# Optimization experiments

Hardware: AMD Instinct MI355X
Metric: run time of the kernel (lower is better)

## Reference

```python
import jax, jax.numpy as jnp
import numpy as np

B = 32768      # batch of graphs
H = 128        # hidden_channels
L = 3          # num message-passing layers
T = 3          # num_timesteps
NB, NJ = 1, 12 # base nodes, joint nodes
NN = NB + NJ   # 13 nodes per graph
OBS_W = 47     # obs features per timestep
BASE_IDX = np.array(list(range(9)) + [45, 46])   # 11 base features per timestep
JOINT_IDX = np.array(list(range(9, 45)))          # 36 joint features per timestep
BASE_F = T * len(BASE_IDX)                        # 33
JOINT_F = (len(JOINT_IDX) // NJ) * T              # 9

# fixed tree edges, both directions (24 edges per graph)
_n2n = np.array([[0, 0, 0, 0, 1, 2, 4, 5, 7, 8, 10, 11],
                 [1, 4, 7, 10, 2, 3, 5, 6, 8, 9, 11, 12]])
SRC = np.concatenate([_n2n[0], _n2n[1]])
DST = np.concatenate([_n2n[1], _n2n[0]])


def setup_inputs() -> dict:
    key = jax.random.key(0)
    ks = jax.random.split(key, 10)
    s = 0.05
    return {
        "obs": jax.random.normal(ks[0], (B, T * OBS_W), dtype=jnp.float32),
        "We_b": jax.random.normal(ks[1], (H, BASE_F), dtype=jnp.float32) * s,
        "be_b": jax.random.normal(ks[2], (H,), dtype=jnp.float32) * s,
        "We_j": jax.random.normal(ks[3], (H, JOINT_F), dtype=jnp.float32) * s,
        "be_j": jax.random.normal(ks[4], (H,), dtype=jnp.float32) * s,
        "W_rel": jax.random.normal(ks[5], (L, H, H), dtype=jnp.float32) * s,
        "W_root": jax.random.normal(ks[6], (L, H, H), dtype=jnp.float32) * s,
        "b_rel": jax.random.normal(ks[7], (L, H), dtype=jnp.float32) * s,
        "W_dec": jax.random.normal(ks[8], (1, H), dtype=jnp.float32) * s,
        "b_dec": jax.random.normal(ks[9], (1,), dtype=jnp.float32) * s,
        "src": jnp.asarray(SRC, dtype=jnp.int32),
        "dst": jnp.asarray(DST, dtype=jnp.int32),
    }


def reference(obs, We_b, be_b, We_j, be_j, W_rel, W_root, b_rel, W_dec, b_dec, src, dst):
    b = obs.shape[0]
    elu = jax.nn.elu
    # ---- obs -> per-node features ----
    obs3 = obs[:, :T * OBS_W].reshape(b, T, OBS_W)
    base_feat = obs3[:, :, BASE_IDX].reshape(b, NB, BASE_F)                 # [B,1,33]
    joint_feat = (obs3[:, :, JOINT_IDX]
                  .reshape(b, T, len(JOINT_IDX) // NJ, NJ)
                  .transpose(0, 3, 1, 2)
                  .reshape(b, NJ, JOINT_F))                                  # [B,12,9]
    # ---- encoders ----
    xb = elu(jnp.einsum('bnf,hf->bnh', base_feat, We_b) + be_b)
    xj = elu(jnp.einsum('bnf,hf->bnh', joint_feat, We_j) + be_j)
    x = jnp.concatenate([xb, xj], axis=1)                                    # [B,13,H]
    # ---- GraphConv layers: out = W_root x + W_rel (scatter_add of x_src at dst) + b ----
    for l in range(L):
        agg = jnp.zeros_like(x).at[:, dst].add(x[:, src])                    # [B,13,H]
        x = elu(jnp.einsum('bnh,oh->bno', agg, W_rel[l]) + b_rel[l]
                + jnp.einsum('bnh,oh->bno', x, W_root[l]))
    # ---- per-joint decoder ----
    out = jnp.einsum('bnh,oh->bno', x[:, NB:], W_dec) + b_dec                # [B,12,1]
    return out.reshape(b, NJ)
```

## Files before the change

kernel.cpp:

```cpp
#include <hip/hip_runtime.h>

#define H      128
#define OBSROW 141
#define GPB    16
#define NT     256

typedef __bf16 bf16x8 __attribute__((ext_vector_type(8)));
typedef float  f32x4  __attribute__((ext_vector_type(4)));

__device__ __forceinline__ float eluf(float v) {
    return v > 0.0f ? v : (__expf(v) - 1.0f);
}
__device__ __forceinline__ f32x4 mf(bf16x8 a, bf16x8 b, f32x4 c) {
    return __builtin_amdgcn_mfma_f32_16x16x32_bf16(a, b, c, 0, 0, 0);
}
__device__ __forceinline__ void store_pk4(unsigned short* dst, f32x4 a) {
    union { unsigned short u[4]; unsigned long long v; } pk;
    #pragma unroll
    for (int r = 0; r < 4; r++) {
        __bf16 b = (__bf16)eluf(a[r]);
        pk.u[r] = *(unsigned short*)&b;
    }
    *(unsigned long long*)dst = pk.v;
}

#define WS_ROOT 49152
#define WS_EB   98304
#define WS_EJ   106496
#define WS_TOT  110592

__global__ void convert_weights(const float* __restrict__ Wr, const float* __restrict__ Wo,
                                const float* __restrict__ Web, const float* __restrict__ Wej,
                                __bf16* __restrict__ ws) {
    const int i = blockIdx.x * 256 + threadIdx.x;
    if (i < WS_ROOT) {
        ws[i] = (__bf16)Wr[i];
    } else if (i < WS_EB) {
        ws[i] = (__bf16)Wo[i - WS_ROOT];
    } else if (i < WS_EJ) {
        const int j = i - WS_EB, o = j >> 6, f = j & 63;
        ws[i] = (__bf16)(f < 33 ? Web[o*33 + f] : 0.0f);
    } else if (i < WS_TOT) {
        const int j = i - WS_EJ, o = j >> 5, f = j & 31;
        ws[i] = (__bf16)(f < 9 ? Wej[o*9 + f] : 0.0f);
    }
}

#define XIDX(n,hc,g,hi) (((((n)*16 + (hc))*16 + (g))*8) + (hi))

__launch_bounds__(NT, 2)
__global__ void gnn_fused(const float* __restrict__ obs,
                          const float* __restrict__ be_b, const float* __restrict__ be_j,
                          const float* __restrict__ b_rel,
                          const float* __restrict__ W_dec, const float* __restrict__ b_dec,
                          const __bf16* __restrict__ wsb,
                          float* __restrict__ out, int B)
{
    __shared__ __align__(16) unsigned short Xs[13*2048];
    __shared__ __align__(16) unsigned short Fs[7168];

    const int tid  = threadIdx.x;
    const int wave = tid >> 6;
    const int lane = tid & 63;
    const int q    = lane >> 4;
    const int c    = lane & 15;
    const int g0   = blockIdx.x * GPB;

    static constexpr int ODEG[13]    = {4,2,2,1,2,2,1,2,2,1,2,2,1};
    static constexpr int ODST[13][4] = {
        {1,4,7,10},{0,2,0,0},{1,3,0,0},{2,0,0,0},{0,5,0,0},{4,6,0,0},{5,0,0,0},
        {0,8,0,0},{7,9,0,0},{8,0,0,0},{0,11,0,0},{10,12,0,0},{11,0,0,0}};

    const int hcs0 = wave*4 + (q>>1);
    const int wofs = c*8 + (q&1)*4;

    {
        float* raw = (float*)Xs;
        for (int i = tid; i < GPB*OBSROW; i += NT) {
            const int g = i / OBSROW;
            raw[i] = ((g0 + g) < B) ? obs[(g0+g)*OBSROW + (i - g*OBSROW)] : 0.0f;
        }
    }
    __syncthreads();

    {
        const float* raw = (const float*)Xs;
        for (int s = tid; s < 6144; s += NT) {
            const int jj = s >> 9, rem = s & 511;
            const int fc = rem >> 7, g = (rem >> 3) & 15, hi = rem & 7;
            const int f = fc*8 + hi;
            float v = 0.0f;
            if (f < 9)
                v = raw[g*OBSROW + (f/3)*47 + 9 + (f%3)*12 + jj];
            *(__bf16*)&Fs[s] = (__bf16)v;
        }
        for (int s = tid; s < 1024; s += NT) {
            const int fc = s >> 7, rem = s & 127, g = rem >> 3, hi = rem & 7;
            const int f = fc*8 + hi;
            float v = 0.0f;
            if (f < 33) {
                const int tt = f / 11, i2 = f % 11;
                v = raw[g*OBSROW + tt*47 + (i2 < 9 ? i2 : 36 + i2)];
            }
            *(__bf16*)&Fs[6144 + s] = (__bf16)v;
        }
    }
    __syncthreads();

    {
        const int orow = wave*32 + c;
        const bf16x8 a0 = *(const bf16x8*)&Fs[6144 + q*128 + c*8];
        const bf16x8 a1 = *(const bf16x8*)&Fs[6144 + 512 + q*128 + c*8];
        #pragma unroll
        for (int s = 0; s < 2; s++) {
            const bf16x8 u0 = *(const bf16x8*)(wsb + WS_EB + (orow + s*16)*64 + q*8);
            const bf16x8 u1 = *(const bf16x8*)(wsb + WS_EB + (orow + s*16)*64 + 32 + q*8);
            const float4 b4 = *(const float4*)&be_b[wave*32 + s*16 + q*4];
            f32x4 acc = {b4.x, b4.y, b4.z, b4.w};
            acc = mf(u0, a0, acc);
            acc = mf(u1, a1, acc);
            store_pk4(&Xs[(hcs0 + s*2)*128 + wofs], acc);
        }
        #pragma unroll
        for (int s = 0; s < 2; s++) {
            const bf16x8 uj = *(const bf16x8*)(wsb + WS_EJ + (orow + s*16)*32 + q*8);
            const float4 b4 = *(const float4*)&be_j[wave*32 + s*16 + q*4];
            const f32x4 bias = {b4.x, b4.y, b4.z, b4.w};
            #pragma unroll
            for (int jj = 0; jj < 12; jj++) {
                const bf16x8 a = *(const bf16x8*)&Fs[jj*512 + q*128 + c*8];
                f32x4 acc = bias;
                acc = mf(uj, a, acc);
                store_pk4(&Xs[(1+jj)*2048 + (hcs0 + s*2)*128 + wofs], acc);
            }
        }
    }
    __syncthreads();

    const unsigned short* xb_base = Xs + q*128 + c*8;
    #pragma unroll 1
    for (int l = 0; l < 3; l++) {
        const __bf16* wr = wsb + l*16384;
        const __bf16* wo = wsb + WS_ROOT + l*16384;
        bf16x8 Wr[2][4], Wt[2][4];
        #pragma unroll
        for (int s = 0; s < 2; s++) {
            const int row = (wave*32 + s*16 + c)*128 + q*8;
            #pragma unroll
            for (int ks = 0; ks < 4; ks++) {
                Wr[s][ks] = *(const bf16x8*)(wr + row + ks*32);
                Wt[s][ks] = *(const bf16x8*)(wo + row + ks*32);
            }
        }
        f32x4 acc[13][2];
        #pragma unroll
        for (int s = 0; s < 2; s++) {
            const float4 b4 = *(const float4*)&b_rel[l*H + wave*32 + s*16 + q*4];
            const f32x4 bias = {b4.x, b4.y, b4.z, b4.w};
            #pragma unroll
            for (int n = 0; n < 13; n++) acc[n][s] = bias;
        }
        #pragma unroll
        for (int n = 0; n < 13; n++) {
            bf16x8 xb[4];
            #pragma unroll
            for (int ks = 0; ks < 4; ks++)
                xb[ks] = *(const bf16x8*)(xb_base + n*2048 + ks*512);
            f32x4 y0 = {0.f,0.f,0.f,0.f}, y1 = {0.f,0.f,0.f,0.f};
            #pragma unroll
            for (int ks = 0; ks < 4; ks++) {
                acc[n][0] = mf(Wt[0][ks], xb[ks], acc[n][0]);
                acc[n][1] = mf(Wt[1][ks], xb[ks], acc[n][1]);
                y0 = mf(Wr[0][ks], xb[ks], y0);
                y1 = mf(Wr[1][ks], xb[ks], y1);
            }
            #pragma unroll
            for (int e = 0; e < 4; e++)
                if (e < ODEG[n]) {
                    acc[ODST[n][e]][0] += y0;
                    acc[ODST[n][e]][1] += y1;
                }
        }
        __syncthreads();
        #pragma unroll
        for (int n = 0; n < 13; n++) {
            store_pk4(&Xs[n*2048 +  hcs0     *128 + wofs], acc[n][0]);
            store_pk4(&Xs[n*2048 + (hcs0 + 2)*128 + wofs], acc[n][1]);
        }
        __syncthreads();
    }

    {
        const unsigned short* xdec = Xs + q*512 + c*8;
        float wd[32];
        #pragma unroll
        for (int i4 = 0; i4 < 8; i4++) {
            const float4 wv = *(const float4*)&W_dec[q*32 + i4*4];
            wd[i4*4+0] = wv.x; wd[i4*4+1] = wv.y; wd[i4*4+2] = wv.z; wd[i4*4+3] = wv.w;
        }
        const float bd = b_dec[0];
        for (int j = wave; j < 12; j += 4) {
            float s = 0.0f;
            #pragma unroll
            for (int hq = 0; hq < 4; hq++) {
                const bf16x8 xv = *(const bf16x8*)(xdec + (j+1)*2048 + hq*128);
                #pragma unroll
                for (int hi2 = 0; hi2 < 8; hi2++)
                    s += (float)xv[hi2] * wd[hq*8 + hi2];
            }
            s += __shfl_xor(s, 16);
            s += __shfl_xor(s, 32);
            if (q == 0 && (g0 + c) < B)
                out[(g0 + c)*12 + j] = s + bd;
        }
    }
}

extern "C" void kernel_launch(void* const* d_in, const int* in_sizes, int n_in,
                              void* d_out, int out_size, void* d_ws, size_t ws_size,
                              hipStream_t stream) {
    const float* obs   = (const float*)d_in[0];
    const float* We_b  = (const float*)d_in[1];
    const float* be_b  = (const float*)d_in[2];
    const float* We_j  = (const float*)d_in[3];
    const float* be_j  = (const float*)d_in[4];
    const float* W_rel = (const float*)d_in[5];
    const float* W_root= (const float*)d_in[6];
    const float* b_rel = (const float*)d_in[7];
    const float* W_dec = (const float*)d_in[8];
    const float* b_dec = (const float*)d_in[9];
    float* out = (float*)d_out;
    __bf16* wsb = (__bf16*)d_ws;

    const int B = in_sizes[0] / OBSROW;
    convert_weights<<<(WS_TOT + 255) / 256, 256, 0, stream>>>(W_rel, W_root, We_b, We_j, wsb);
    const int blocks = (B + GPB - 1) / GPB;
    gnn_fused<<<blocks, NT, 0, stream>>>(obs, be_b, be_j, b_rel, W_dec, b_dec,
                                         wsb, out, B);
}
```

Baseline: 208.5 us.

## Alias feature staging buffer into node buffer to allow three blocks per CU

Drops the separate feature LDS buffer and stages the encoder inputs inside the tail of the node-feature buffer, lowering shared memory per block. Launch bounds go from 2 to 3 blocks per CU so more blocks can be resident. Because the joint encoder outputs for the last nodes overlap the staging area, their results are kept in registers, an extra barrier is added, and they are written back afterwards. The costs are higher register pressure from the held accumulators and a tighter register budget under the new launch bound, which may cause spills.

```diff
diff --git a/kernel.cpp b/kernel.cpp
--- a/kernel.cpp
+++ b/kernel.cpp
@@ -46,9 +46,9 @@
     }
 }
 
-#define XIDX(n,hc,g,hi) (((((n)*16 + (hc))*16 + (g))*8) + (hi))
-
-__launch_bounds__(NT, 2)
+#define G0U 19456
+
+__launch_bounds__(NT, 3)
 __global__ void gnn_fused(const float* __restrict__ obs,
                           const float* __restrict__ be_b, const float* __restrict__ be_j,
                           const float* __restrict__ b_rel,
@@ -57,7 +57,6 @@
                           float* __restrict__ out, int B)
 {
     __shared__ __align__(16) unsigned short Xs[13*2048];
-    __shared__ __align__(16) unsigned short Fs[7168];
 
     const int tid  = threadIdx.x;
     const int wave = tid >> 6;
@@ -92,7 +91,7 @@
             float v = 0.0f;
             if (f < 9)
                 v = raw[g*OBSROW + (f/3)*47 + 9 + (f%3)*12 + jj];
-            *(__bf16*)&Fs[s] = (__bf16)v;
+            *(__bf16*)&Xs[G0U + s] = (__bf16)v;
         }
         for (int s = tid; s < 1024; s += NT) {
             const int fc = s >> 7, rem = s & 127, g = rem >> 3, hi = rem & 7;
@@ -102,15 +101,15 @@
                 const int tt = f / 11, i2 = f % 11;
                 v = raw[g*OBSROW + tt*47 + (i2 < 9 ? i2 : 36 + i2)];
             }
-            *(__bf16*)&Fs[6144 + s] = (__bf16)v;
+            *(__bf16*)&Xs[G0U + 6144 + s] = (__bf16)v;
         }
     }
     __syncthreads();
 
     {
         const int orow = wave*32 + c;
-        const bf16x8 a0 = *(const bf16x8*)&Fs[6144 + q*128 + c*8];
-        const bf16x8 a1 = *(const bf16x8*)&Fs[6144 + 512 + q*128 + c*8];
+        const bf16x8 a0 = *(const bf16x8*)&Xs[G0U + 6144 + q*128 + c*8];
+        const bf16x8 a1 = *(const bf16x8*)&Xs[G0U + 6144 + 512 + q*128 + c*8];
         #pragma unroll
         for (int s = 0; s < 2; s++) {
             const bf16x8 u0 = *(const bf16x8*)(wsb + WS_EB + (orow + s*16)*64 + q*8);
@@ -121,18 +120,33 @@
             acc = mf(u1, a1, acc);
             store_pk4(&Xs[(hcs0 + s*2)*128 + wofs], acc);
         }
-        #pragma unroll
-        for (int s = 0; s < 2; s++) {
-            const bf16x8 uj = *(const bf16x8*)(wsb + WS_EJ + (orow + s*16)*32 + q*8);
+        bf16x8 uj[2];
+        f32x4 bias[2];
+        #pragma unroll
+        for (int s = 0; s < 2; s++) {
+            uj[s] = *(const bf16x8*)(wsb + WS_EJ + (orow + s*16)*32 + q*8);
             const float4 b4 = *(const float4*)&be_j[wave*32 + s*16 + q*4];
-            const f32x4 bias = {b4.x, b4.y, b4.z, b4.w};
-            #pragma unroll
-            for (int jj = 0; jj < 12; jj++) {
-                const bf16x8 a = *(const bf16x8*)&Fs[jj*512 + q*128 + c*8];
-                f32x4 acc = bias;
-                acc = mf(uj, a, acc);
-                store_pk4(&Xs[(1+jj)*2048 + (hcs0 + s*2)*128 + wofs], acc);
-            }
+            bias[s] = (f32x4){b4.x, b4.y, b4.z, b4.w};
+        }
+        f32x4 dacc[2][4];
+        #pragma unroll
+        for (int jj = 0; jj < 12; jj++) {
+            const bf16x8 a = *(const bf16x8*)&Xs[G0U + jj*512 + q*128 + c*8];
+            #pragma unroll
+            for (int s = 0; s < 2; s++) {
+                f32x4 acc = bias[s];
+                acc = mf(uj[s], a, acc);
+                if (jj < 8)
+                    store_pk4(&Xs[(1+jj)*2048 + (hcs0 + s*2)*128 + wofs], acc);
+                else
+                    dacc[s][jj-8] = acc;
+            }
+        }
+        __syncthreads();
+        #pragma unroll
+        for (int t = 0; t < 4; t++) {
+            store_pk4(&Xs[(9+t)*2048 +  hcs0     *128 + wofs], dacc[0][t]);
+            store_pk4(&Xs[(9+t)*2048 + (hcs0+2)  *128 + wofs], dacc[1][t]);
         }
     }
     __syncthreads();
```

Result: slower. 217.0 us (+4.0%).
